# Optimization experiments

Measured on AMD Instinct MI355X. Metric: run time of the kernel, lower is better.

Reference implementation:

```python
import jax, jax.numpy as jnp
import numpy as np
from jax import lax

B, G, P = 16, 128, 8000   # batch, MAX_GT_BOXES, num proposals
R = 200                   # train_rois_per_image
POS_CAP = int(R * 0.33)   # max positive rois per image = 66
BOX_STD = np.array([0.1, 0.1, 0.2, 0.2], np.float32)


def _make_boxes(k, shape):
    k1, k2, k3, k4 = jax.random.split(k, 4)
    y1 = jax.random.uniform(k1, shape) * 0.6
    x1 = jax.random.uniform(k2, shape) * 0.6
    h = jax.random.uniform(k3, shape) * 0.35 + 0.02
    w = jax.random.uniform(k4, shape) * 0.35 + 0.02
    return jnp.stack([y1, x1, y1 + h, x1 + w], axis=-1)


def setup_inputs() -> dict:
    key = jax.random.key(0)
    kg, kp, kc, kn, km = jax.random.split(key, 5)
    gt4 = _make_boxes(kg, (B, G))
    gt_cnt = jax.random.randint(kc, (B,), 5, G + 1)
    gt_tag = jnp.arange(G)[None, :] < gt_cnt[:, None]
    gt_boxes = jnp.concatenate([gt4, gt_tag[..., None].astype(jnp.float32)], axis=-1)
    cls = jax.random.randint(kn, (B, G), 1, 81)
    gt_class_ids = jnp.stack([cls * gt_tag, gt_tag.astype(jnp.int32)], axis=-1).astype(jnp.int32)
    pr4 = _make_boxes(kp, (B, P))
    pr_cnt = jax.random.randint(km, (B,), P // 2, P + 1)
    pr_tag = jnp.arange(P)[None, :] < pr_cnt[:, None]
    proposals = jnp.concatenate([pr4, pr_tag[..., None].astype(jnp.float32)], axis=-1)
    return {"gt_boxes": gt_boxes, "gt_class_ids": gt_class_ids, "proposals": proposals}


def _iou(gtb, prb):
    # gtb [G,4], prb [P,4] -> [G,P]
    iw = jnp.maximum(0.0, jnp.minimum(gtb[:, None, 3], prb[None, :, 3]) - jnp.maximum(gtb[:, None, 1], prb[None, :, 1]))
    ih = jnp.maximum(0.0, jnp.minimum(gtb[:, None, 2], prb[None, :, 2]) - jnp.maximum(gtb[:, None, 0], prb[None, :, 0]))
    inter = iw * ih
    ag = (gtb[:, 3] - gtb[:, 1]) * (gtb[:, 2] - gtb[:, 0])
    ap = (prb[:, 3] - prb[:, 1]) * (prb[:, 2] - prb[:, 0])
    return inter / (ag[:, None] + ap[None, :] - inter)


def _regress_target(anchors, gt):
    h = anchors[:, 2] - anchors[:, 0]
    w = anchors[:, 3] - anchors[:, 1]
    gh = gt[:, 2] - gt[:, 0]
    gw = gt[:, 3] - gt[:, 1]
    cy = (anchors[:, 2] + anchors[:, 0]) * 0.5
    cx = (anchors[:, 3] + anchors[:, 1]) * 0.5
    gcy = (gt[:, 2] + gt[:, 0]) * 0.5
    gcx = (gt[:, 3] + gt[:, 1]) * 0.5
    dy = (gcy - cy) / h
    dx = (gcx - cx) / w
    dh = jnp.log(jnp.maximum(gh / h, 1e-8))
    dw = jnp.log(jnp.maximum(gw / w, 1e-8))
    return jnp.stack([dy, dx, dh, dw], axis=1) / jnp.asarray(BOX_STD)


def _detect_targets_one(key, gt_boxes, gt_cls, proposals):
    valid_gt = gt_boxes[:, 4] != 0
    valid_pr = proposals[:, 4] != 0
    gtb = gt_boxes[:, :4]
    prb = proposals[:, :4]
    iou = jnp.where(valid_gt[:, None] & valid_pr[None, :], _iou(gtb, prb), -1.0)
    # remove each GT's best proposal from the candidate set (setdiff1d in original)
    gt_argmax = jnp.argmax(iou, axis=1)
    removed = jnp.zeros(P, jnp.int32).at[gt_argmax].max(valid_gt.astype(jnp.int32)) > 0
    iou2 = jnp.where(removed[None, :], -1.0, iou)
    p_max = iou2.max(axis=0)
    p_arg = jnp.argmax(iou2, axis=0)
    keep = (~removed) & valid_pr
    pos_m = keep & (p_max >= 0.5)
    neg_m = keep & (p_max < 0.5)
    # random subsampling (tf.random_shuffle) via uniform scores + top_k
    k1, k2 = jax.random.split(key)
    pos_idx = lax.top_k(jnp.where(pos_m, jax.random.uniform(k1, (P,)), -1.0), POS_CAP)[1]
    neg_idx = lax.top_k(jnp.where(neg_m, jax.random.uniform(k2, (P,)), -1.0), R)[1]
    n_pos = jnp.minimum(pos_m.sum(), POS_CAP)
    n_neg = jnp.minimum(R - n_pos, neg_m.sum())
    slot = jnp.arange(R)
    is_pos = slot < n_pos
    is_real = slot < n_pos + n_neg
    idx = jnp.where(is_pos, pos_idx[jnp.minimum(slot, POS_CAP - 1)], neg_idx[jnp.clip(slot - n_pos, 0, R - 1)])
    rois4 = jnp.where(is_real[:, None], prb[idx], 0.0)
    gsel = p_arg[idx]
    deltas4 = jnp.where(is_pos[:, None], _regress_target(prb[idx], gtb[gsel]), 0.0)
    cls = jnp.where(is_pos, gt_cls[gsel, 0].astype(jnp.float32), 0.0)
    delta_tag = jnp.where(is_pos, 1.0, jnp.where(is_real, -1.0, 0.0))
    deltas = jnp.concatenate([deltas4, delta_tag[:, None]], axis=1)      # [R,5]
    class_ids = jnp.stack([cls, is_real.astype(jnp.float32)], axis=1)    # [R,2]
    rois = jnp.concatenate([rois4, is_real[:, None].astype(jnp.float32)], axis=1)  # [R,5]
    matched = jnp.zeros(G, jnp.int32).at[p_arg].max(pos_m.astype(jnp.int32))
    miss = (valid_gt.sum() - (matched * valid_gt.astype(jnp.int32)).sum()).astype(jnp.float32)
    return deltas, class_ids, rois, miss


def reference(gt_boxes, gt_class_ids, proposals):
    keys = jax.random.split(jax.random.key(42), gt_boxes.shape[0])
    return jax.vmap(_detect_targets_one)(keys, gt_boxes, gt_class_ids, proposals)
```

## Files before the change

### kernel.cpp

```cpp
#include <hip/hip_runtime.h>
#include <stdint.h>

#define Bn 16
#define Gn 128
#define Pn 8000
#define Rn 200
#define POSCAP 66
#define CANDN 512
#define SLICES 32
#define TILE 250

typedef unsigned long long u64;

__device__ __forceinline__ void tf2x32(uint32_t k0, uint32_t k1,
                                       uint32_t x0, uint32_t x1,
                                       uint32_t& y0, uint32_t& y1) {
  uint32_t ks0 = k0, ks1 = k1, ks2 = k0 ^ k1 ^ 0x1BD11BDAu;
  x0 += ks0; x1 += ks1;
#define TF_ROUND(r) { x0 += x1; x1 = (x1 << (r)) | (x1 >> (32 - (r))); x1 ^= x0; }
  TF_ROUND(13) TF_ROUND(15) TF_ROUND(26) TF_ROUND(6)
  x0 += ks1; x1 += ks2 + 1u;
  TF_ROUND(17) TF_ROUND(29) TF_ROUND(16) TF_ROUND(24)
  x0 += ks2; x1 += ks0 + 2u;
  TF_ROUND(13) TF_ROUND(15) TF_ROUND(26) TF_ROUND(6)
  x0 += ks0; x1 += ks1 + 3u;
  TF_ROUND(17) TF_ROUND(29) TF_ROUND(16) TF_ROUND(24)
  x0 += ks1; x1 += ks2 + 4u;
  TF_ROUND(13) TF_ROUND(15) TF_ROUND(26) TF_ROUND(6)
  x0 += ks2; x1 += ks0 + 5u;
#undef TF_ROUND
  y0 = x0; y1 = x1;
}

__device__ __forceinline__ float iou_f(float g0, float g1, float g2, float g3, float ag,
                                       float p0, float p1, float p2, float p3) {
  float iw = fmaxf(0.0f, __fsub_rn(fminf(g3, p3), fmaxf(g1, p1)));
  float ih = fmaxf(0.0f, __fsub_rn(fminf(g2, p2), fmaxf(g0, p0)));
  float inter = __fmul_rn(iw, ih);
  float ap = __fmul_rn(__fsub_rn(p3, p1), __fsub_rn(p2, p0));
  return __fdiv_rn(inter, __fsub_rn(__fadd_rn(ag, ap), inter));
}

__global__ __launch_bounds__(256) void k_phase1(const float* __restrict__ gt,
                                                const float* __restrict__ pr,
                                                uint16_t* __restrict__ combo,
                                                u64* __restrict__ rowpk2) {
  __shared__ float sp[TILE * 5];
  __shared__ float sg[Gn * 5];
  int blk = blockIdx.x;
  int b = blk >> 5, s = blk & 31;
  int tid = threadIdx.x;
  const float* prb = pr + ((size_t)b * Pn + s * TILE) * 5;
  for (int i = tid; i < TILE * 5; i += 256) sp[i] = prb[i];
  for (int i = tid; i < Gn * 5; i += 256) sg[i] = gt[(size_t)b * Gn * 5 + i];
  __syncthreads();

  if (tid < TILE) {
    float p0 = sp[tid * 5], p1 = sp[tid * 5 + 1], p2 = sp[tid * 5 + 2];
    float p3 = sp[tid * 5 + 3], pv = sp[tid * 5 + 4];
    int prelim = 0, bidx = 0;
    if (pv != 0.0f) {
      float best = -2.0f;
      for (int g = 0; g < Gn; g++) {
        float gv = sg[g * 5 + 4];
        if (gv != 0.0f) {
          float g0 = sg[g * 5], g1 = sg[g * 5 + 1], g2 = sg[g * 5 + 2], g3 = sg[g * 5 + 3];
          float ag = __fmul_rn(__fsub_rn(g3, g1), __fsub_rn(g2, g0));
          float v = iou_f(g0, g1, g2, g3, ag, p0, p1, p2, p3);
          if (v > best) { best = v; bidx = g; }
        }
      }
      prelim = (best >= 0.5f) ? 2 : 1;
    }
    combo[(size_t)b * Pn + s * TILE + tid] = (uint16_t)((prelim << 8) | bidx);
  }

  int wave = tid >> 6, lane = tid & 63;
  for (int gi = 0; gi < 32; gi++) {
    int g = wave * 32 + gi;
    float gv = sg[g * 5 + 4];
    u64 key = 0;
    if (gv != 0.0f) {
      float g0 = sg[g * 5], g1 = sg[g * 5 + 1], g2 = sg[g * 5 + 2], g3 = sg[g * 5 + 3];
      float ag = __fmul_rn(__fsub_rn(g3, g1), __fsub_rn(g2, g0));
#pragma unroll
      for (int k = 0; k < 4; k++) {
        int p = lane + k * 64;
        if (p < TILE) {
          float pv = sp[p * 5 + 4];
          if (pv != 0.0f) {
            float v = iou_f(g0, g1, g2, g3, ag, sp[p * 5], sp[p * 5 + 1],
                            sp[p * 5 + 2], sp[p * 5 + 3]);
            u64 kk = ((u64)__float_as_uint(v) << 32) | (unsigned)(~(s * TILE + p));
            if (kk > key) key = kk;
          }
        }
      }
      for (int off = 32; off > 0; off >>= 1) {
        u64 o = __shfl_down(key, off);
        if (o > key) key = o;
      }
    }
    if (lane == 0) rowpk2[((size_t)b * SLICES + s) * Gn + g] = key;
  }
}

__global__ __launch_bounds__(1024) void k_select(
    const float* __restrict__ gt, const int* __restrict__ gtc,
    const float* __restrict__ pr, const uint16_t* __restrict__ combo,
    const u64* __restrict__ rowpk2, float* __restrict__ out) {
  __shared__ uint32_t skey[Pn];
  __shared__ uint32_t hist2[1024];
  __shared__ uint32_t hist1[1024];
  __shared__ u64 cand[CANDN];
  __shared__ uint32_t rembm[Pn / 32 + 1];
  __shared__ int matched[Gn];
  __shared__ int s_npos, s_nneg, s_miss, s_call, s_cpos, s_T2, s_T1;
  __shared__ uint32_t s_keys[4];
  int b = blockIdx.x, tid = threadIdx.x;

  hist2[tid] = 0; hist1[tid] = 0;
  if (tid < CANDN) cand[tid] = 0ull;
  if (tid < Pn / 32 + 1) rembm[tid] = 0;
  if (tid < Gn) matched[tid] = 0;
  if (tid == 0) {
    s_npos = 0; s_nneg = 0; s_miss = 0; s_call = 0; s_cpos = 0;
    s_T2 = 1025; s_T1 = 1025;
    uint32_t kb0, kb1, a0, a1, c0, c1;
    tf2x32(0u, 42u, 0u, (uint32_t)b, kb0, kb1);
    tf2x32(kb0, kb1, 0u, 0u, a0, a1);
    tf2x32(kb0, kb1, 0u, 1u, c0, c1);
    s_keys[0] = a0; s_keys[1] = a1; s_keys[2] = c0; s_keys[3] = c1;
  }
  __syncthreads();

  if (tid < Gn) {
    u64 m = 0;
    const u64* rp = rowpk2 + (size_t)b * SLICES * Gn + tid;
#pragma unroll 8
    for (int sl = 0; sl < SLICES; sl++) {
      u64 v = rp[sl * Gn];
      if (v > m) m = v;
    }
    if (m != 0ull) {
      unsigned p = ~(unsigned)(m & 0xFFFFFFFFull);
      atomicOr(&rembm[p >> 5], 1u << (p & 31));
    }
  }
  __syncthreads();

  uint32_t k10 = s_keys[0], k11 = s_keys[1], k20 = s_keys[2], k21 = s_keys[3];
  const size_t bp = (size_t)b * Pn;
  int lpos = 0, lneg = 0;
  for (int p = tid; p < Pn; p += 1024) {
    uint32_t cb = combo[bp + p];
    int rem = (rembm[p >> 5] >> (p & 31)) & 1;
    int cls = rem ? 0 : (int)(cb >> 8);
    uint32_t key = 0;
    if (cls) {
      uint32_t kk0 = (cls == 2) ? k10 : k20, kk1 = (cls == 2) ? k11 : k21;
      uint32_t y0, y1;
      tf2x32(kk0, kk1, 0u, (uint32_t)p, y0, y1);
      uint32_t val = (y0 ^ y1) >> 9;
      key = ((uint32_t)cls << 23) | val;
      if (cls == 2) { lpos++; matched[cb & 127] = 1; atomicAdd(&hist2[val >> 13], 1u); }
      else { lneg++; atomicAdd(&hist1[val >> 13], 1u); }
    }
    skey[p] = key;
  }
  if (lpos) atomicAdd(&s_npos, lpos);
  if (lneg) atomicAdd(&s_nneg, lneg);
  __syncthreads();

  if (tid < 128) {
    bool isP = tid < 64;
    int lane = tid & 63;
    uint32_t* hist = isP ? hist2 : hist1;
    int cnt = isP ? s_npos : s_nneg;
    int cap = isP ? POSCAP : Rn;
    int need = cnt < cap ? cnt : cap;
    int base = 1024 - 16 * (lane + 1);
    int local = 0;
#pragma unroll
    for (int j = 0; j < 16; j++) local += (int)hist[base + j];
    int incl = local;
    for (int d = 1; d < 64; d <<= 1) {
      int o = __shfl_up(incl, d);
      if (lane >= d) incl += o;
    }
    int above = incl - local;
    if (need > 0 && above < need && above + local >= need) {
      int cum = above, T = base;
      for (int j = 15; j >= 0; j--) {
        cum += (int)hist[base + j];
        if (cum >= need) { T = base + j; break; }
      }
      if (isP) s_T2 = T; else s_T1 = T;
    }
  }
  __syncthreads();
  int T2 = s_T2, T1 = s_T1;

  for (int p = tid; p < Pn; p += 1024) {
    uint32_t key = skey[p];
    int cls = (int)(key >> 23);
    if (cls) {
      int bucket = (int)((key & 0x7FFFFFu) >> 13);
      int T = (cls == 2) ? T2 : T1;
      if (bucket >= T) {
        int slot = atomicAdd(&s_call, 1);
        if (slot < CANDN) {
          cand[slot] = ((u64)key << 16) | (uint32_t)((uint16_t)(~p));
          if (cls == 2) atomicAdd(&s_cpos, 1);
        }
      }
    }
  }
  __syncthreads();

  for (unsigned k = 2; k <= CANDN; k <<= 1) {
    for (unsigned j = k >> 1; j > 0; j >>= 1) {
      unsigned i = tid, l = i ^ j;
      if (i < CANDN && l > i) {
        u64 av = cand[i], cv = cand[l];
        bool a_first = av > cv;
        bool desc = ((i & k) == 0u);
        if (desc != a_first) { cand[i] = cv; cand[l] = av; }
      }
      __syncthreads();
    }
  }

  int npos = s_npos, nneg = s_nneg, cpos = s_cpos;
  int n_pos = npos < POSCAP ? npos : POSCAP;
  int rems = Rn - n_pos;
  int n_neg = nneg < rems ? nneg : rems;

  float* o_del = out;
  float* o_cls = out + (size_t)Bn * Rn * 5;
  float* o_roi = out + (size_t)Bn * Rn * 7;
  float* o_mis = out + (size_t)Bn * Rn * 12;

  if (tid < Rn) {
    int s = tid;
    bool is_pos = s < n_pos;
    bool is_real = s < n_pos + n_neg;
    float d0 = 0, d1 = 0, d2 = 0, d3 = 0, d4 = 0, c0 = 0, c1 = 0;
    float r0 = 0, r1 = 0, r2 = 0, r3 = 0, r4 = 0;
    if (is_real) {
      int ci = is_pos ? s : (cpos + (s - n_pos));
      u64 ck = cand[ci];
      int p = (int)((~(unsigned)ck) & 0xFFFFu);
      const float* pb = pr + (bp + p) * 5;
      float q0 = pb[0], q1 = pb[1], q2 = pb[2], q3 = pb[3];
      r0 = q0; r1 = q1; r2 = q2; r3 = q3; r4 = 1.0f; c1 = 1.0f;
      if (is_pos) {
        int g = (int)(combo[bp + p] & 127);
        const float* gb = gt + ((size_t)b * Gn + g) * 5;
        float g0 = gb[0], g1 = gb[1], g2 = gb[2], g3 = gb[3];
        float h = __fsub_rn(q2, q0), w = __fsub_rn(q3, q1);
        float gh = __fsub_rn(g2, g0), gw = __fsub_rn(g3, g1);
        float cy = __fmul_rn(__fadd_rn(q2, q0), 0.5f);
        float cx = __fmul_rn(__fadd_rn(q3, q1), 0.5f);
        float gcy = __fmul_rn(__fadd_rn(g2, g0), 0.5f);
        float gcx = __fmul_rn(__fadd_rn(g3, g1), 0.5f);
        float dy = __fdiv_rn(__fsub_rn(gcy, cy), h);
        float dx = __fdiv_rn(__fsub_rn(gcx, cx), w);
        float dh = logf(fmaxf(__fdiv_rn(gh, h), 1e-8f));
        float dw = logf(fmaxf(__fdiv_rn(gw, w), 1e-8f));
        d0 = __fdiv_rn(dy, 0.1f); d1 = __fdiv_rn(dx, 0.1f);
        d2 = __fdiv_rn(dh, 0.2f); d3 = __fdiv_rn(dw, 0.2f);
        d4 = 1.0f;
        c0 = (float)gtc[((size_t)b * Gn + g) * 2];
      } else {
        d4 = -1.0f;
      }
    }
    size_t ob = (size_t)b * Rn + s;
    o_del[ob * 5 + 0] = d0; o_del[ob * 5 + 1] = d1; o_del[ob * 5 + 2] = d2;
    o_del[ob * 5 + 3] = d3; o_del[ob * 5 + 4] = d4;
    o_cls[ob * 2 + 0] = c0; o_cls[ob * 2 + 1] = c1;
    o_roi[ob * 5 + 0] = r0; o_roi[ob * 5 + 1] = r1; o_roi[ob * 5 + 2] = r2;
    o_roi[ob * 5 + 3] = r3; o_roi[ob * 5 + 4] = r4;
  }

  if (tid < Gn) {
    float gv = gt[((size_t)b * Gn + tid) * 5 + 4];
    if (gv != 0.0f && matched[tid] == 0) atomicAdd(&s_miss, 1);
  }
  __syncthreads();
  if (tid == 0) o_mis[b] = (float)s_miss;
}

extern "C" void kernel_launch(void* const* d_in, const int* in_sizes, int n_in,
                              void* d_out, int out_size, void* d_ws, size_t ws_size,
                              hipStream_t stream) {
  const float* gt = (const float*)d_in[0];
  const int* gtc = (const int*)d_in[1];
  const float* pr = (const float*)d_in[2];
  float* out = (float*)d_out;

  u64* rowpk2 = (u64*)d_ws;
  uint16_t* combo = (uint16_t*)(rowpk2 + Bn * SLICES * Gn);

  k_phase1<<<Bn * SLICES, 256, 0, stream>>>(gt, pr, combo, rowpk2);
  k_select<<<Bn, 1024, 0, stream>>>(gt, gtc, pr, combo, rowpk2, out);
}
```

Before: 138.3 us.

## Split IoU phase into half-size tiles with padded float4 boxes and parallel slice reduction

Doubles the slice count so each phase-1 block handles 125 proposals, which gives twice as many blocks. Box data is stored padded to 8 floats with a precomputed area, and invalid boxes are marked with a NaN area so the validity branches disappear. Waves are specialised: two waves compute the per-GT max over proposals in registers, replacing the shuffle reduction, while the other two compute the per-proposal argmax. In the select kernel, the per-GT max across slices is now reduced by all 1024 threads in parallel instead of by 128 threads in serial. The risks are more rowpk2 traffic and NaN-based masking that must keep the same tie-breaking and results.

```diff
diff --git a/kernel.cpp b/kernel.cpp
--- a/kernel.cpp
+++ b/kernel.cpp
@@ -7,8 +7,8 @@
 #define Rn 200
 #define POSCAP 66
 #define CANDN 512
-#define SLICES 32
-#define TILE 250
+#define SLICES 64
+#define TILE 125
 
 typedef unsigned long long u64;
 
@@ -32,76 +32,75 @@
   y0 = x0; y1 = x1;
 }
 
-__device__ __forceinline__ float iou_f(float g0, float g1, float g2, float g3, float ag,
-                                       float p0, float p1, float p2, float p3) {
-  float iw = fmaxf(0.0f, __fsub_rn(fminf(g3, p3), fmaxf(g1, p1)));
-  float ih = fmaxf(0.0f, __fsub_rn(fminf(g2, p2), fmaxf(g0, p0)));
+__device__ __forceinline__ float iou_pk(const float4& g, float ga,
+                                        const float4& p, float pa) {
+  float iw = fmaxf(0.0f, __fsub_rn(fminf(g.w, p.w), fmaxf(g.y, p.y)));
+  float ih = fmaxf(0.0f, __fsub_rn(fminf(g.z, p.z), fmaxf(g.x, p.x)));
   float inter = __fmul_rn(iw, ih);
-  float ap = __fmul_rn(__fsub_rn(p3, p1), __fsub_rn(p2, p0));
-  return __fdiv_rn(inter, __fsub_rn(__fadd_rn(ag, ap), inter));
+  return __fdiv_rn(inter, __fsub_rn(__fadd_rn(ga, pa), inter));
 }
 
 __global__ __launch_bounds__(256) void k_phase1(const float* __restrict__ gt,
                                                 const float* __restrict__ pr,
                                                 uint16_t* __restrict__ combo,
                                                 u64* __restrict__ rowpk2) {
-  __shared__ float sp[TILE * 5];
-  __shared__ float sg[Gn * 5];
+  __shared__ __align__(16) float sp[TILE * 8];
+  __shared__ __align__(16) float sg[Gn * 8];
   int blk = blockIdx.x;
-  int b = blk >> 5, s = blk & 31;
+  int b = blk >> 6, s = blk & 63;
   int tid = threadIdx.x;
-  const float* prb = pr + ((size_t)b * Pn + s * TILE) * 5;
-  for (int i = tid; i < TILE * 5; i += 256) sp[i] = prb[i];
-  for (int i = tid; i < Gn * 5; i += 256) sg[i] = gt[(size_t)b * Gn * 5 + i];
-  __syncthreads();
+  const float kNaN = __uint_as_float(0x7FC00000u);
 
   if (tid < TILE) {
-    float p0 = sp[tid * 5], p1 = sp[tid * 5 + 1], p2 = sp[tid * 5 + 2];
-    float p3 = sp[tid * 5 + 3], pv = sp[tid * 5 + 4];
-    int prelim = 0, bidx = 0;
-    if (pv != 0.0f) {
-      float best = -2.0f;
+    const float* pb = pr + ((size_t)b * Pn + s * TILE + tid) * 5;
+    float c0 = pb[0], c1 = pb[1], c2 = pb[2], c3 = pb[3], v = pb[4];
+    float area = __fmul_rn(__fsub_rn(c3, c1), __fsub_rn(c2, c0));
+    if (v == 0.0f) area = kNaN;
+    sp[tid * 8 + 0] = c0; sp[tid * 8 + 1] = c1; sp[tid * 8 + 2] = c2;
+    sp[tid * 8 + 3] = c3; sp[tid * 8 + 4] = area;
+  } else if (tid >= 128) {
+    int g = tid - 128;
+    const float* gb = gt + ((size_t)b * Gn + g) * 5;
+    float c0 = gb[0], c1 = gb[1], c2 = gb[2], c3 = gb[3], v = gb[4];
+    float area = __fmul_rn(__fsub_rn(c3, c1), __fsub_rn(c2, c0));
+    if (v == 0.0f) area = kNaN;
+    sg[g * 8 + 0] = c0; sg[g * 8 + 1] = c1; sg[g * 8 + 2] = c2;
+    sg[g * 8 + 3] = c3; sg[g * 8 + 4] = area;
+  }
+  __syncthreads();
+
+  int wave = tid >> 6, lane = tid & 63;
+  if (wave < 2) {
+    int g = (wave << 6) | lane;
+    float4 gb = *(const float4*)&sg[g * 8];
+    float ga = sg[g * 8 + 4];
+    float best = -2.0f; int bestp = -1;
+    for (int p = 0; p < TILE; p++) {
+      float4 pb = *(const float4*)&sp[p * 8];
+      float pa = sp[p * 8 + 4];
+      float v = iou_pk(gb, ga, pb, pa);
+      if (v > best) { best = v; bestp = p; }
+    }
+    u64 key = 0;
+    if (bestp >= 0)
+      key = ((u64)__float_as_uint(best) << 32) | (unsigned)(~(s * TILE + bestp));
+    rowpk2[((size_t)b * SLICES + s) * Gn + g] = key;
+  } else {
+    int t2 = tid - 128;
+    if (t2 < TILE) {
+      float4 pb = *(const float4*)&sp[t2 * 8];
+      float pa = sp[t2 * 8 + 4];
+      float best = -2.0f; int bestg = -1;
       for (int g = 0; g < Gn; g++) {
-        float gv = sg[g * 5 + 4];
-        if (gv != 0.0f) {
-          float g0 = sg[g * 5], g1 = sg[g * 5 + 1], g2 = sg[g * 5 + 2], g3 = sg[g * 5 + 3];
-          float ag = __fmul_rn(__fsub_rn(g3, g1), __fsub_rn(g2, g0));
-          float v = iou_f(g0, g1, g2, g3, ag, p0, p1, p2, p3);
-          if (v > best) { best = v; bidx = g; }
-        }
-      }
-      prelim = (best >= 0.5f) ? 2 : 1;
-    }
-    combo[(size_t)b * Pn + s * TILE + tid] = (uint16_t)((prelim << 8) | bidx);
-  }
-
-  int wave = tid >> 6, lane = tid & 63;
-  for (int gi = 0; gi < 32; gi++) {
-    int g = wave * 32 + gi;
-    float gv = sg[g * 5 + 4];
-    u64 key = 0;
-    if (gv != 0.0f) {
-      float g0 = sg[g * 5], g1 = sg[g * 5 + 1], g2 = sg[g * 5 + 2], g3 = sg[g * 5 + 3];
-      float ag = __fmul_rn(__fsub_rn(g3, g1), __fsub_rn(g2, g0));
-#pragma unroll
-      for (int k = 0; k < 4; k++) {
-        int p = lane + k * 64;
-        if (p < TILE) {
-          float pv = sp[p * 5 + 4];
-          if (pv != 0.0f) {
-            float v = iou_f(g0, g1, g2, g3, ag, sp[p * 5], sp[p * 5 + 1],
-                            sp[p * 5 + 2], sp[p * 5 + 3]);
-            u64 kk = ((u64)__float_as_uint(v) << 32) | (unsigned)(~(s * TILE + p));
-            if (kk > key) key = kk;
-          }
-        }
-      }
-      for (int off = 32; off > 0; off >>= 1) {
-        u64 o = __shfl_down(key, off);
-        if (o > key) key = o;
-      }
-    }
-    if (lane == 0) rowpk2[((size_t)b * SLICES + s) * Gn + g] = key;
+        float4 gb = *(const float4*)&sg[g * 8];
+        float ga = sg[g * 8 + 4];
+        float v = iou_pk(gb, ga, pb, pa);
+        if (v > best) { best = v; bestg = g; }
+      }
+      int cls = 0, pa_out = 0;
+      if (bestg >= 0) { cls = (best >= 0.5f) ? 2 : 1; pa_out = bestg; }
+      combo[(size_t)b * Pn + s * TILE + t2] = (uint16_t)((cls << 8) | pa_out);
+    }
   }
 }
 
@@ -113,12 +112,24 @@
   __shared__ uint32_t hist2[1024];
   __shared__ uint32_t hist1[1024];
   __shared__ u64 cand[CANDN];
+  __shared__ u64 pm8[1024];
   __shared__ uint32_t rembm[Pn / 32 + 1];
   __shared__ int matched[Gn];
   __shared__ int s_npos, s_nneg, s_miss, s_call, s_cpos, s_T2, s_T1;
   __shared__ uint32_t s_keys[4];
   int b = blockIdx.x, tid = threadIdx.x;
 
+  {
+    int g = tid >> 3, c = tid & 7;
+    const u64* base = rowpk2 + (size_t)b * SLICES * Gn + g;
+    u64 m = 0;
+#pragma unroll
+    for (int i = 0; i < 8; i++) {
+      u64 v = base[(size_t)(c * 8 + i) * Gn];
+      if (v > m) m = v;
+    }
+    pm8[tid] = m;
+  }
   hist2[tid] = 0; hist1[tid] = 0;
   if (tid < CANDN) cand[tid] = 0ull;
   if (tid < Pn / 32 + 1) rembm[tid] = 0;
@@ -136,10 +147,9 @@
 
   if (tid < Gn) {
     u64 m = 0;
-    const u64* rp = rowpk2 + (size_t)b * SLICES * Gn + tid;
-#pragma unroll 8
-    for (int sl = 0; sl < SLICES; sl++) {
-      u64 v = rp[sl * Gn];
+#pragma unroll
+    for (int i = 0; i < 8; i++) {
+      u64 v = pm8[tid * 8 + i];
       if (v > m) m = v;
     }
     if (m != 0ull) {
```

After: 113.7 us. 1.22x faster.
